# Optimization experiments

Measured on AMD Instinct MI355X. Metric: run time of the kernel, lower is better.

The kernel has to match this reference:

```python
import jax, jax.numpy as jnp
import numpy as np

MASK_NUM = -2.0**32 + 1.0  # additive masking constant from the original layer


def setup_inputs() -> dict:
    key = jax.random.key(0)
    k1, k2, k3, k4 = jax.random.split(key, 4)
    BH, S, D = 32, 2048, 64  # batch*heads, seq_len, head_dim
    B = 4                    # original batch (masks are per-batch, tiled by heads)
    queries = jax.random.normal(k1, (BH, S, D), dtype=jnp.float32)
    keys_ = jax.random.normal(k2, (BH, S, D), dtype=jnp.float32)
    values = jax.random.normal(k3, (BH, S, D), dtype=jnp.float32)
    masks = jax.random.randint(k4, (B, S), 0, 2, dtype=jnp.int32)
    return {"queries": queries, "keys": keys_, "values": values, "masks": masks}


def reference(queries, keys, values, masks):
    BH, S, D = queries.shape
    # scores = Q K^T / sqrt(D)   -> [BH, S, S]
    scores = jnp.einsum("bqd,bkd->bqk", queries, keys) / (D ** 0.5)
    # key-padding mask: masks [B, S] tiled along axis 0 by BH // B, broadcast over query dim
    reps = BH // masks.shape[0]
    m = jnp.tile(masks.astype(jnp.float32), (reps, 1))[:, None, :]  # [BH, 1, S]
    scores = scores + m * MASK_NUM
    # causal (future) mask: keep lower triangle, replace rest with MASK_NUM
    tril = jnp.tril(jnp.ones((S, S), dtype=jnp.float32))
    scores = jnp.where(tril == 0, jnp.float32(MASK_NUM), scores)
    attn = jax.nn.softmax(scores, axis=-1)
    # dropout_rate = 0.0 -> identity
    return jnp.einsum("bqk,bkd->bqd", attn, values)
```

## Files before the change

### kernel.cpp

```cpp
#include <hip/hip_runtime.h>

#define S_LEN 2048
#define HDIM  64
#define NHEAD 32
#define NBATCH 4
#define QBLK 64
#define KBLK 64
#define QK_SCALE (0.125f * 1.44269504088896341f)

typedef float f32x4 __attribute__((ext_vector_type(4)));
typedef short bf16x8 __attribute__((ext_vector_type(8)));

static __device__ __forceinline__ unsigned int cvt_pk_bf16(float lo, float hi) {
    unsigned int r;
    asm("v_cvt_pk_bf16_f32 %0, %1, %2" : "=v"(r) : "v"(lo), "v"(hi));
    return r;
}

__global__ void maskprep_kernel(const int* __restrict__ masks,
                                int* __restrict__ Lb,
                                unsigned long long* __restrict__ MB) {
    const int b = blockIdx.x;
    const int t = threadIdx.x;
    __shared__ int smin;
    if (t == 0) smin = S_LEN;
    __syncthreads();
    int local = S_LEN;
    for (int k = t; k < S_LEN; k += 64) {
        if (masks[b * S_LEN + k] == 0) { local = k; break; }
    }
    atomicMin(&smin, local);
    if (t < 32) {
        unsigned long long wbits = 0ull;
        for (int i = 0; i < 64; ++i)
            wbits |= (unsigned long long)(masks[b * S_LEN + t * 64 + i] & 1) << i;
        MB[b * 32 + t] = wbits;
    }
    __syncthreads();
    if (t == 0) Lb[b] = smin;
}

__global__ void meanv_kernel(const float* __restrict__ V, float* __restrict__ meanV) {
    const int bh = blockIdx.x;
    const int t = threadIdx.x;
    const int d = t & 63;
    const int part = t >> 6;
    const float* Vb = V + (size_t)bh * S_LEN * HDIM;
    float s = 0.f;
    const int k0 = part * (S_LEN / 4);
    for (int k = k0; k < k0 + S_LEN / 4; ++k) s += Vb[(size_t)k * HDIM + d];
    __shared__ float red[4][64];
    red[part][d] = s;
    __syncthreads();
    if (t < 64) {
        float tot = red[0][t] + red[1][t] + red[2][t] + red[3][t];
        meanV[bh * HDIM + t] = tot * (1.0f / (float)S_LEN);
    }
}

#define P_OFF 32768
#define LDSB  40960

__global__ __launch_bounds__(256) void attn_fwd(
    const float* __restrict__ Q, const float* __restrict__ K,
    const float* __restrict__ V, const float* __restrict__ meanV,
    const int* __restrict__ Lb, const unsigned long long* __restrict__ MB,
    float* __restrict__ out)
{
    __shared__ __align__(16) char lds[LDSB];
    const int tid  = threadIdx.x;
    const int lane = tid & 63;
    const int w    = tid >> 6;
    const int lq   = lane & 15;
    const int lk   = lane >> 4;

    const int bid  = blockIdx.x;
    const int nbid = (bid & 7) * 128 + (bid >> 3);
    const int bh   = nbid >> 5;
    const int qb   = 31 - (nbid & 31);
    const int q0   = qb * QBLK;
    const int b    = bh & (NBATCH - 1);
    const int nt   = qb + 1;

    const size_t ho = (size_t)bh * S_LEN * HDIM;
    const float* Qh = Q + ho;
    const float* Kh = K + ho;
    const float* Vh = V + ho;

    bf16x8 qf[2];
    {
        const float* qrow = Qh + (size_t)(q0 + w * 16 + lq) * HDIM;
        #pragma unroll
        for (int c = 0; c < 2; ++c) {
            const int d0 = lk * 8 + c * 32;
            float4 f0 = *(const float4*)(qrow + d0);
            float4 f1 = *(const float4*)(qrow + d0 + 4);
            int4 qi;
            qi.x = cvt_pk_bf16(f0.x * QK_SCALE, f0.y * QK_SCALE);
            qi.y = cvt_pk_bf16(f0.z * QK_SCALE, f0.w * QK_SCALE);
            qi.z = cvt_pk_bf16(f1.x * QK_SCALE, f1.y * QK_SCALE);
            qi.w = cvt_pk_bf16(f1.z * QK_SCALE, f1.w * QK_SCALE);
            qf[c] = *(bf16x8*)&qi;
        }
    }

    const int kr = tid >> 2;
    const int kc = (tid & 3) << 4;
    const float* Kp = Kh + (size_t)kr * HDIM + kc;
    const int vd = lane;
    const int vk = w * 16;
    const float* Vp = Vh + (size_t)vk * HDIM + vd;

    float4 ka0, ka1, ka2, ka3;
    float va[16];

    auto LOADKV = [&](int kk0) {
        const float4* kp = (const float4*)(Kp + (size_t)kk0 * HDIM);
        ka0 = kp[0]; ka1 = kp[1]; ka2 = kp[2]; ka3 = kp[3];
        const float* vp = Vp + (size_t)kk0 * HDIM;
        #pragma unroll
        for (int i = 0; i < 16; ++i) va[i] = vp[i * HDIM];
    };
    auto WRITEKV = [&](int bufbase) {
        int4 kv0, kv1;
        kv0.x = cvt_pk_bf16(ka0.x, ka0.y); kv0.y = cvt_pk_bf16(ka0.z, ka0.w);
        kv0.z = cvt_pk_bf16(ka1.x, ka1.y); kv0.w = cvt_pk_bf16(ka1.z, ka1.w);
        kv1.x = cvt_pk_bf16(ka2.x, ka2.y); kv1.y = cvt_pk_bf16(ka2.z, ka2.w);
        kv1.z = cvt_pk_bf16(ka3.x, ka3.y); kv1.w = cvt_pk_bf16(ka3.z, ka3.w);
        const int kswz = (kr & 7) << 4;
        *(int4*)&lds[bufbase + ((kr * 128 + kc * 2)      ^ kswz)] = kv0;
        *(int4*)&lds[bufbase + ((kr * 128 + kc * 2 + 16) ^ kswz)] = kv1;
        int4 vv0, vv1;
        vv0.x = cvt_pk_bf16(va[0],  va[1]);  vv0.y = cvt_pk_bf16(va[2],  va[3]);
        vv0.z = cvt_pk_bf16(va[4],  va[5]);  vv0.w = cvt_pk_bf16(va[6],  va[7]);
        vv1.x = cvt_pk_bf16(va[8],  va[9]);  vv1.y = cvt_pk_bf16(va[10], va[11]);
        vv1.z = cvt_pk_bf16(va[12], va[13]); vv1.w = cvt_pk_bf16(va[14], va[15]);
        const int vswz = (vd & 7) << 4;
        *(int4*)&lds[bufbase + 8192 + ((vd * 128 + vk * 2)      ^ vswz)] = vv0;
        *(int4*)&lds[bufbase + 8192 + ((vd * 128 + vk * 2 + 16) ^ vswz)] = vv1;
    };

    f32x4 acc[4];
    #pragma unroll
    for (int g = 0; g < 4; ++g) acc[g] = (f32x4){0.f, 0.f, 0.f, 0.f};
    float m_r = -__builtin_inff();
    float l_r = 0.f;

    const int swz = (lq & 7) << 4;
    const int pbase = P_OFF + (w << 11);
    const int wq = w * 16 + lq;

    LOADKV(0);
    WRITEKV(0);
    __syncthreads();

    for (int t = 0; t < nt; ++t) {
        const int cur = t & 1;
        const int kb  = cur << 14;
        const bool pre = (t + 1) < nt;
        if (pre) LOADKV((t + 1) * KBLK);

        f32x4 sacc[4];
        #pragma unroll
        for (int g = 0; g < 4; ++g) sacc[g] = (f32x4){0.f, 0.f, 0.f, 0.f};
        #pragma unroll
        for (int c = 0; c < 2; ++c) {
            #pragma unroll
            for (int g = 0; g < 4; ++g) {
                bf16x8 kf = *(const bf16x8*)&lds[kb + (((16 * g + lq) * 128 + 16 * lk + 64 * c) ^ swz)];
                sacc[g] = __builtin_amdgcn_mfma_f32_16x16x32_bf16(kf, qf[c], sacc[g], 0, 0, 0);
            }
        }

        const unsigned long long mb = MB[(b << 5) + t];
        const bool diag = (t == nt - 1);

        float mloc = sacc[0][0];
        #pragma unroll
        for (int g = 0; g < 4; ++g)
            #pragma unroll
            for (int r = 0; r < 4; ++r) mloc = fmaxf(mloc, sacc[g][r]);
        mloc = fmaxf(mloc, __shfl_xor(mloc, 16, 64));
        mloc = fmaxf(mloc, __shfl_xor(mloc, 32, 64));
        const float newm = fmaxf(m_r, mloc);
        const float sc = exp2f(m_r - newm);

        float ls = 0.f;
        #pragma unroll
        for (int g = 0; g < 4; ++g) {
            const unsigned int nib = (unsigned int)(mb >> (16 * g + 4 * lk)) & 0xFu;
            #pragma unroll
            for (int r = 0; r < 4; ++r) {
                const int kidx = 16 * g + 4 * lk + r;
                float e = exp2f(sacc[g][r] - newm);
                const bool kill = ((nib >> r) & 1u) || (diag && kidx > wq);
                e = kill ? 0.f : e;
                sacc[g][r] = e;
                ls += e;
            }
        }
        ls += __shfl_xor(ls, 16, 64);
        ls += __shfl_xor(ls, 32, 64);
        l_r = l_r * sc + ls;
        m_r = newm;

        float scb[4];
        #pragma unroll
        for (int r = 0; r < 4; ++r) scb[r] = __shfl(sc, 4 * lk + r, 64);
        #pragma unroll
        for (int g = 0; g < 4; ++g)
            #pragma unroll
            for (int r = 0; r < 4; ++r) acc[g][r] *= scb[r];

        #pragma unroll
        for (int g = 0; g < 4; ++g) {
            uint2 pw;
            pw.x = cvt_pk_bf16(sacc[g][0], sacc[g][1]);
            pw.y = cvt_pk_bf16(sacc[g][2], sacc[g][3]);
            *(uint2*)&lds[pbase + ((lq * 128 + 32 * g + 8 * lk) ^ swz)] = pw;
        }

        #pragma unroll
        for (int c = 0; c < 2; ++c) {
            bf16x8 pa = *(const bf16x8*)&lds[pbase + ((lq * 128 + 16 * lk + 64 * c) ^ swz)];
            #pragma unroll
            for (int g = 0; g < 4; ++g) {
                bf16x8 vb = *(const bf16x8*)&lds[kb + 8192 + (((lq + 16 * g) * 128 + 16 * lk + 64 * c) ^ swz)];
                acc[g] = __builtin_amdgcn_mfma_f32_16x16x32_bf16(pa, vb, acc[g], 0, 0, 0);
            }
        }

        if (pre) WRITEKV((cur ^ 1) << 14);
        __syncthreads();
    }

    const int myL = Lb[b];
    const float linv_s = 1.0f / l_r;
    float linv[4];
    #pragma unroll
    for (int r = 0; r < 4; ++r) linv[r] = __shfl(linv_s, 4 * lk + r, 64);
    #pragma unroll
    for (int r = 0; r < 4; ++r) {
        const int qrow = q0 + w * 16 + 4 * lk + r;
        float* orow = out + ho + (size_t)qrow * HDIM;
        if (qrow < myL) {
            #pragma unroll
            for (int g = 0; g < 4; ++g) orow[lq + 16 * g] = meanV[bh * HDIM + lq + 16 * g];
        } else {
            #pragma unroll
            for (int g = 0; g < 4; ++g) orow[lq + 16 * g] = acc[g][r] * linv[r];
        }
    }
}

extern "C" void kernel_launch(void* const* d_in, const int* in_sizes, int n_in,
                              void* d_out, int out_size, void* d_ws, size_t ws_size,
                              hipStream_t stream)
{
    const float* Q     = (const float*)d_in[0];
    const float* K     = (const float*)d_in[1];
    const float* V     = (const float*)d_in[2];
    const int*   masks = (const int*)d_in[3];
    float* out = (float*)d_out;

    float* meanV = (float*)d_ws;
    int*   Lb    = (int*)((char*)d_ws + 8192);
    unsigned long long* MB = (unsigned long long*)((char*)d_ws + 8208);

    maskprep_kernel<<<dim3(NBATCH), dim3(64), 0, stream>>>(masks, Lb, MB);
    meanv_kernel<<<dim3(NHEAD), dim3(256), 0, stream>>>(V, meanV);
    attn_fwd<<<dim3(1024), dim3(256), 0, stream>>>(Q, K, V, meanV, Lb, MB, out);
}
```

Measured before the change: 180.4 us.

## Pre-convert K/V to swizzled bf16, DMA to LDS, pair causal q-blocks

A separate kernel now converts K and V once to swizzled bf16 tile images in the workspace and computes meanV with atomics. The attention kernel stages those images straight into LDS with global_load_lds instead of loading fp32 per block and converting it. Each workgroup processes a short and a long causal q-block (j and 31-j) to balance work across 512 blocks. It also skips the softmax rescale when the running max grows by less than a threshold, raises wave priority around the MFMAs, and picks fully masked rows by l==0 instead of a prefix length. The costs are an extra pass over K and V, more workspace, and dependence on the workspace size for the fast path.

After: 155.5 us. 13.8% less time.

```diff
diff --git a/kernel.cpp b/kernel.cpp
--- a/kernel.cpp
+++ b/kernel.cpp
@@ -1,4 +1,5 @@
 #include <hip/hip_runtime.h>
+#include <stdint.h>
 
 #define S_LEN 2048
 #define HDIM  64
@@ -7,9 +8,17 @@
 #define QBLK 64
 #define KBLK 64
 #define QK_SCALE (0.125f * 1.44269504088896341f)
+#define DEFER_THR 8.0f
 
 typedef float f32x4 __attribute__((ext_vector_type(4)));
 typedef short bf16x8 __attribute__((ext_vector_type(8)));
+
+#define WS_MEANV 0
+#define WS_MB    8192
+#define WS_KBF   16384
+#define KVBYTES  (NHEAD * 32 * 8192)
+#define WS_VTBF  (WS_KBF + (size_t)KVBYTES)
+#define WS_NEED_PRE (WS_VTBF + (size_t)KVBYTES)
 
 static __device__ __forceinline__ unsigned int cvt_pk_bf16(float lo, float hi) {
     unsigned int r;
@@ -17,54 +26,101 @@
     return r;
 }
 
+static __device__ __forceinline__ void load_lds16(const void* g, void* l) {
+    __builtin_amdgcn_global_load_lds(
+        (const __attribute__((address_space(1))) uint32_t*)g,
+        (__attribute__((address_space(3))) uint32_t*)l, 16, 0, 0);
+}
+
 __global__ void maskprep_kernel(const int* __restrict__ masks,
-                                int* __restrict__ Lb,
                                 unsigned long long* __restrict__ MB) {
     const int b = blockIdx.x;
-    const int t = threadIdx.x;
-    __shared__ int smin;
-    if (t == 0) smin = S_LEN;
-    __syncthreads();
-    int local = S_LEN;
-    for (int k = t; k < S_LEN; k += 64) {
-        if (masks[b * S_LEN + k] == 0) { local = k; break; }
-    }
-    atomicMin(&smin, local);
-    if (t < 32) {
-        unsigned long long wbits = 0ull;
-        for (int i = 0; i < 64; ++i)
-            wbits |= (unsigned long long)(masks[b * S_LEN + t * 64 + i] & 1) << i;
-        MB[b * 32 + t] = wbits;
-    }
-    __syncthreads();
-    if (t == 0) Lb[b] = smin;
-}
-
-__global__ void meanv_kernel(const float* __restrict__ V, float* __restrict__ meanV) {
-    const int bh = blockIdx.x;
-    const int t = threadIdx.x;
-    const int d = t & 63;
-    const int part = t >> 6;
+    const int lane = threadIdx.x & 63;
+    const int w = threadIdx.x >> 6;
+    #pragma unroll
+    for (int i = 0; i < 8; ++i) {
+        const int word = i * 4 + w;
+        const int m = masks[b * S_LEN + word * 64 + lane];
+        const unsigned long long bits = __ballot(m != 0);
+        if (lane == 0) MB[b * 32 + word] = bits;
+    }
+}
+
+__global__ void meanv_atomic_kernel(const float* __restrict__ V, float* __restrict__ meanV) {
+    const int bh = blockIdx.x >> 3, part = blockIdx.x & 7;
+    const int t = threadIdx.x, d = t & 63, sub = t >> 6;
     const float* Vb = V + (size_t)bh * S_LEN * HDIM;
     float s = 0.f;
-    const int k0 = part * (S_LEN / 4);
-    for (int k = k0; k < k0 + S_LEN / 4; ++k) s += Vb[(size_t)k * HDIM + d];
+    const int k0 = part * 256 + sub * 64;
+    for (int k = k0; k < k0 + 64; ++k) s += Vb[(size_t)k * HDIM + d];
     __shared__ float red[4][64];
-    red[part][d] = s;
+    red[sub][d] = s;
     __syncthreads();
     if (t < 64) {
         float tot = red[0][t] + red[1][t] + red[2][t] + red[3][t];
-        meanV[bh * HDIM + t] = tot * (1.0f / (float)S_LEN);
+        atomicAdd(&meanV[bh * HDIM + t], tot * (1.0f / (float)S_LEN));
+    }
+}
+
+__global__ __launch_bounds__(256) void cvt_kernel(
+    const float* __restrict__ K, const float* __restrict__ V,
+    uint8_t* __restrict__ Kbf, uint8_t* __restrict__ Vtbf,
+    float* __restrict__ meanV)
+{
+    const int bh = blockIdx.x >> 5, t = blockIdx.x & 31;
+    const int tid = threadIdx.x, lane = tid & 63, w = tid >> 6;
+    const size_t ho = (size_t)bh * S_LEN * HDIM;
+    const size_t img = ((size_t)bh * 32 + t) * 8192;
+
+    {
+        const int kr = tid >> 2;
+        const int kc = (tid & 3) << 4;
+        const float4* kp = (const float4*)(K + ho + (size_t)(t * 64 + kr) * HDIM + kc);
+        float4 a0 = kp[0], a1 = kp[1], a2 = kp[2], a3 = kp[3];
+        int4 kv0, kv1;
+        kv0.x = cvt_pk_bf16(a0.x, a0.y); kv0.y = cvt_pk_bf16(a0.z, a0.w);
+        kv0.z = cvt_pk_bf16(a1.x, a1.y); kv0.w = cvt_pk_bf16(a1.z, a1.w);
+        kv1.x = cvt_pk_bf16(a2.x, a2.y); kv1.y = cvt_pk_bf16(a2.z, a2.w);
+        kv1.z = cvt_pk_bf16(a3.x, a3.y); kv1.w = cvt_pk_bf16(a3.z, a3.w);
+        const int swz = (kr & 7) << 4;
+        *(int4*)&Kbf[img + ((kr * 128 + kc * 2)      ^ swz)] = kv0;
+        *(int4*)&Kbf[img + ((kr * 128 + kc * 2 + 16) ^ swz)] = kv1;
+    }
+    {
+        const int vd = lane;
+        const int vk = w * 16;
+        const float* vp = V + ho + (size_t)(t * 64 + vk) * HDIM + vd;
+        float va[16];
+        float psum = 0.f;
+        #pragma unroll
+        for (int i = 0; i < 16; ++i) { va[i] = vp[(size_t)i * HDIM]; psum += va[i]; }
+        int4 vv0, vv1;
+        vv0.x = cvt_pk_bf16(va[0],  va[1]);  vv0.y = cvt_pk_bf16(va[2],  va[3]);
+        vv0.z = cvt_pk_bf16(va[4],  va[5]);  vv0.w = cvt_pk_bf16(va[6],  va[7]);
+        vv1.x = cvt_pk_bf16(va[8],  va[9]);  vv1.y = cvt_pk_bf16(va[10], va[11]);
+        vv1.z = cvt_pk_bf16(va[12], va[13]); vv1.w = cvt_pk_bf16(va[14], va[15]);
+        const int swz = (vd & 7) << 4;
+        *(int4*)&Vtbf[img + ((vd * 128 + vk * 2)      ^ swz)] = vv0;
+        *(int4*)&Vtbf[img + ((vd * 128 + vk * 2 + 16) ^ swz)] = vv1;
+        __shared__ float red[4][64];
+        red[w][vd] = psum;
+        __syncthreads();
+        if (tid < 64) {
+            float tot = red[0][tid] + red[1][tid] + red[2][tid] + red[3][tid];
+            atomicAdd(&meanV[bh * HDIM + tid], tot * (1.0f / (float)S_LEN));
+        }
     }
 }
 
 #define P_OFF 32768
 #define LDSB  40960
 
+template<bool PRE>
 __global__ __launch_bounds__(256) void attn_fwd(
     const float* __restrict__ Q, const float* __restrict__ K,
     const float* __restrict__ V, const float* __restrict__ meanV,
-    const int* __restrict__ Lb, const unsigned long long* __restrict__ MB,
+    const unsigned long long* __restrict__ MB,
+    const uint8_t* __restrict__ Kbf, const uint8_t* __restrict__ Vtbf,
     float* __restrict__ out)
 {
     __shared__ __align__(16) char lds[LDSB];
@@ -75,51 +131,41 @@
     const int lk   = lane >> 4;
 
     const int bid  = blockIdx.x;
-    const int nbid = (bid & 7) * 128 + (bid >> 3);
-    const int bh   = nbid >> 5;
-    const int qb   = 31 - (nbid & 31);
-    const int q0   = qb * QBLK;
+    const int nbid = (bid & 7) * 64 + (bid >> 3);
+    const int bh   = nbid >> 4;
+    const int j    = nbid & 15;
     const int b    = bh & (NBATCH - 1);
-    const int nt   = qb + 1;
 
     const size_t ho = (size_t)bh * S_LEN * HDIM;
     const float* Qh = Q + ho;
     const float* Kh = K + ho;
     const float* Vh = V + ho;
-
-    bf16x8 qf[2];
-    {
-        const float* qrow = Qh + (size_t)(q0 + w * 16 + lq) * HDIM;
-        #pragma unroll
-        for (int c = 0; c < 2; ++c) {
-            const int d0 = lk * 8 + c * 32;
-            float4 f0 = *(const float4*)(qrow + d0);
-            float4 f1 = *(const float4*)(qrow + d0 + 4);
-            int4 qi;
-            qi.x = cvt_pk_bf16(f0.x * QK_SCALE, f0.y * QK_SCALE);
-            qi.y = cvt_pk_bf16(f0.z * QK_SCALE, f0.w * QK_SCALE);
-            qi.z = cvt_pk_bf16(f1.x * QK_SCALE, f1.y * QK_SCALE);
-            qi.w = cvt_pk_bf16(f1.z * QK_SCALE, f1.w * QK_SCALE);
-            qf[c] = *(bf16x8*)&qi;
-        }
-    }
+    const uint8_t* kimg = Kbf  + (size_t)bh * 32 * 8192;
+    const uint8_t* vimg = Vtbf + (size_t)bh * 32 * 8192;
 
     const int kr = tid >> 2;
     const int kc = (tid & 3) << 4;
-    const float* Kp = Kh + (size_t)kr * HDIM + kc;
     const int vd = lane;
     const int vk = w * 16;
+    const float* Kp = Kh + (size_t)kr * HDIM + kc;
     const float* Vp = Vh + (size_t)vk * HDIM + vd;
-
     float4 ka0, ka1, ka2, ka3;
     float va[16];
 
+    auto STAGE = [&](int t, int bufbase) {
+        const uint8_t* gk = kimg + (size_t)t * 8192 + w * 2048 + lane * 16;
+        const uint8_t* gv = vimg + (size_t)t * 8192 + w * 2048 + lane * 16;
+        load_lds16(gk,        &lds[bufbase + w * 2048]);
+        load_lds16(gk + 1024, &lds[bufbase + w * 2048 + 1024]);
+        load_lds16(gv,        &lds[bufbase + 8192 + w * 2048]);
+        load_lds16(gv + 1024, &lds[bufbase + 8192 + w * 2048 + 1024]);
+    };
     auto LOADKV = [&](int kk0) {
         const float4* kp = (const float4*)(Kp + (size_t)kk0 * HDIM);
         ka0 = kp[0]; ka1 = kp[1]; ka2 = kp[2]; ka3 = kp[3];
         const float* vp = Vp + (size_t)kk0 * HDIM;
         #pragma unroll
-        for (int i = 0; i < 16; ++i) va[i] = vp[i * HDIM];
+        for (int i = 0; i < 16; ++i) va[i] = vp[(size_t)i * HDIM];
     };
     auto WRITEKV = [&](int bufbase) {
         int4 kv0, kv1;
@@ -140,115 +186,146 @@
         *(int4*)&lds[bufbase + 8192 + ((vd * 128 + vk * 2 + 16) ^ vswz)] = vv1;
     };
 
-    f32x4 acc[4];
-    #pragma unroll
-    for (int g = 0; g < 4; ++g) acc[g] = (f32x4){0.f, 0.f, 0.f, 0.f};
-    float m_r = -__builtin_inff();
-    float l_r = 0.f;
-
     const int swz = (lq & 7) << 4;
     const int pbase = P_OFF + (w << 11);
     const int wq = w * 16 + lq;
 
-    LOADKV(0);
-    WRITEKV(0);
-    __syncthreads();
-
-    for (int t = 0; t < nt; ++t) {
-        const int cur = t & 1;
-        const int kb  = cur << 14;
-        const bool pre = (t + 1) < nt;
-        if (pre) LOADKV((t + 1) * KBLK);
-
-        f32x4 sacc[4];
-        #pragma unroll
-        for (int g = 0; g < 4; ++g) sacc[g] = (f32x4){0.f, 0.f, 0.f, 0.f};
-        #pragma unroll
-        for (int c = 0; c < 2; ++c) {
+    #pragma unroll 1
+    for (int pass = 0; pass < 2; ++pass) {
+        const int qb = pass ? (31 - j) : j;
+        const int q0 = qb * QBLK;
+        const int nt = qb + 1;
+
+        bf16x8 qf[2];
+        {
+            const float* qrow = Qh + (size_t)(q0 + w * 16 + lq) * HDIM;
+            #pragma unroll
+            for (int c = 0; c < 2; ++c) {
+                const int d0 = lk * 8 + c * 32;
+                float4 f0 = *(const float4*)(qrow + d0);
+                float4 f1 = *(const float4*)(qrow + d0 + 4);
+                int4 qi;
+                qi.x = cvt_pk_bf16(f0.x * QK_SCALE, f0.y * QK_SCALE);
+                qi.y = cvt_pk_bf16(f0.z * QK_SCALE, f0.w * QK_SCALE);
+                qi.z = cvt_pk_bf16(f1.x * QK_SCALE, f1.y * QK_SCALE);
+                qi.w = cvt_pk_bf16(f1.z * QK_SCALE, f1.w * QK_SCALE);
+                qf[c] = *(bf16x8*)&qi;
+            }
+        }
+
+        f32x4 acc[4];
+        #pragma unroll
+        for (int g = 0; g < 4; ++g) acc[g] = (f32x4){0.f, 0.f, 0.f, 0.f};
+        float m_r = -__builtin_inff();
+        float l_r = 0.f;
+
+        if constexpr (PRE) STAGE(0, 0);
+        else { LOADKV(0); WRITEKV(0); }
+        __syncthreads();
+
+        for (int t = 0; t < nt; ++t) {
+            const int cur = t & 1;
+            const int kb  = cur << 14;
+            const bool pre = (t + 1) < nt;
+            if constexpr (PRE) { if (pre) STAGE(t + 1, (cur ^ 1) << 14); }
+            else               { if (pre) LOADKV((t + 1) * KBLK); }
+
+            f32x4 sacc[4];
+            #pragma unroll
+            for (int g = 0; g < 4; ++g) sacc[g] = (f32x4){0.f, 0.f, 0.f, 0.f};
+            __builtin_amdgcn_s_setprio(1);
+            #pragma unroll
+            for (int c = 0; c < 2; ++c) {
+                #pragma unroll
+                for (int g = 0; g < 4; ++g) {
+                    bf16x8 kf = *(const bf16x8*)&lds[kb + (((16 * g + lq) * 128 + 16 * lk + 64 * c) ^ swz)];
+                    sacc[g] = __builtin_amdgcn_mfma_f32_16x16x32_bf16(kf, qf[c], sacc[g], 0, 0, 0);
+                }
+            }
+            __builtin_amdgcn_s_setprio(0);
+
+            const unsigned long long mb = MB[(b << 5) + t];
+            const bool diag = (t == nt - 1);
+
+            float mloc = sacc[0][0];
+            #pragma unroll
+            for (int g = 0; g < 4; ++g)
+                #pragma unroll
+                for (int r = 0; r < 4; ++r) mloc = fmaxf(mloc, sacc[g][r]);
+            mloc = fmaxf(mloc, __shfl_xor(mloc, 16, 64));
+            mloc = fmaxf(mloc, __shfl_xor(mloc, 32, 64));
+
+            if (!__all(mloc - m_r <= DEFER_THR)) {
+                const float newm = fmaxf(m_r, mloc);
+                const float sc = exp2f(m_r - newm);
+                l_r *= sc;
+                m_r = newm;
+                float scb[4];
+                #pragma unroll
+                for (int r = 0; r < 4; ++r) scb[r] = __shfl(sc, 4 * lk + r, 64);
+                #pragma unroll
+                for (int g = 0; g < 4; ++g)
+                    #pragma unroll
+                    for (int r = 0; r < 4; ++r) acc[g][r] *= scb[r];
+            }
+
+            float ls = 0.f;
             #pragma unroll
             for (int g = 0; g < 4; ++g) {
-                bf16x8 kf = *(const bf16x8*)&lds[kb + (((16 * g + lq) * 128 + 16 * lk + 64 * c) ^ swz)];
-                sacc[g] = __builtin_amdgcn_mfma_f32_16x16x32_bf16(kf, qf[c], sacc[g], 0, 0, 0);
-            }
+                const unsigned int nib = (unsigned int)(mb >> (16 * g + 4 * lk)) & 0xFu;
+                #pragma unroll
+                for (int r = 0; r < 4; ++r) {
+                    const int kidx = 16 * g + 4 * lk + r;
+                    float e = exp2f(sacc[g][r] - m_r);
+                    const bool kill = ((nib >> r) & 1u) || (diag && kidx > wq);
+                    e = kill ? 0.f : e;
+                    sacc[g][r] = e;
+                    ls += e;
+                }
+            }
+            ls += __shfl_xor(ls, 16, 64);
+            ls += __shfl_xor(ls, 32, 64);
+            l_r += ls;
+
+            #pragma unroll
+            for (int g = 0; g < 4; ++g) {
+                uint2 pw;
+                pw.x = cvt_pk_bf16(sacc[g][0], sacc[g][1]);
+                pw.y = cvt_pk_bf16(sacc[g][2], sacc[g][3]);
+                *(uint2*)&lds[pbase + ((lq * 128 + 32 * g + 8 * lk) ^ swz)] = pw;
+            }
+
+            __builtin_amdgcn_s_setprio(1);
+            #pragma unroll
+            for (int c = 0; c < 2; ++c) {
+                bf16x8 pa = *(const bf16x8*)&lds[pbase + ((lq * 128 + 16 * lk + 64 * c) ^ swz)];
+                #pragma unroll
+                for (int g = 0; g < 4; ++g) {
+                    bf16x8 vb = *(const bf16x8*)&lds[kb + 8192 + (((lq + 16 * g) * 128 + 16 * lk + 64 * c) ^ swz)];
+                    acc[g] = __builtin_amdgcn_mfma_f32_16x16x32_bf16(pa, vb, acc[g], 0, 0, 0);
+                }
+            }
+            __builtin_amdgcn_s_setprio(0);
+
+            if constexpr (!PRE) { if (pre) WRITEKV((cur ^ 1) << 14); }
+            __syncthreads();
         }
 
-        const unsigned long long mb = MB[(b << 5) + t];
-        const bool diag = (t == nt - 1);
-
-        float mloc = sacc[0][0];
-        #pragma unroll
-        for (int g = 0; g < 4; ++g)
-            #pragma unroll
-            for (int r = 0; r < 4; ++r) mloc = fmaxf(mloc, sacc[g][r]);
-        mloc = fmaxf(mloc, __shfl_xor(mloc, 16, 64));
-        mloc = fmaxf(mloc, __shfl_xor(mloc, 32, 64));
-        const float newm = fmaxf(m_r, mloc);
-        const float sc = exp2f(m_r - newm);
-
-        float ls = 0.f;
-        #pragma unroll
-        for (int g = 0; g < 4; ++g) {
-            const unsigned int nib = (unsigned int)(mb >> (16 * g + 4 * lk)) & 0xFu;
-            #pragma unroll
-            for (int r = 0; r < 4; ++r) {
-                const int kidx = 16 * g + 4 * lk + r;
-                float e = exp2f(sacc[g][r] - newm);
-                const bool kill = ((nib >> r) & 1u) || (diag && kidx > wq);
-                e = kill ? 0.f : e;
-                sacc[g][r] = e;
-                ls += e;
-            }
-        }
-        ls += __shfl_xor(ls, 16, 64);
-        ls += __shfl_xor(ls, 32, 64);
-        l_r = l_r * sc + ls;
-        m_r = newm;
-
-        float scb[4];
-        #pragma unroll
-        for (int r = 0; r < 4; ++r) scb[r] = __shfl(sc, 4 * lk + r, 64);
-        #pragma unroll
-        for (int g = 0; g < 4; ++g)
-            #pragma unroll
-            for (int r = 0; r < 4; ++r) acc[g][r] *= scb[r];
-
-        #pragma unroll
-        for (int g = 0; g < 4; ++g) {
-            uint2 pw;
-            pw.x = cvt_pk_bf16(sacc[g][0], sacc[g][1]);
-            pw.y = cvt_pk_bf16(sacc[g][2], sacc[g][3]);
-            *(uint2*)&lds[pbase + ((lq * 128 + 32 * g + 8 * lk) ^ swz)] = pw;
-        }
-
-        #pragma unroll
-        for (int c = 0; c < 2; ++c) {
-            bf16x8 pa = *(const bf16x8*)&lds[pbase + ((lq * 128 + 16 * lk + 64 * c) ^ swz)];
-            #pragma unroll
-            for (int g = 0; g < 4; ++g) {
-                bf16x8 vb = *(const bf16x8*)&lds[kb + 8192 + (((lq + 16 * g) * 128 + 16 * lk + 64 * c) ^ swz)];
-                acc[g] = __builtin_amdgcn_mfma_f32_16x16x32_bf16(pa, vb, acc[g], 0, 0, 0);
-            }
-        }
-
-        if (pre) WRITEKV((cur ^ 1) << 14);
-        __syncthreads();
-    }
-
-    const int myL = Lb[b];
-    const float linv_s = 1.0f / l_r;
-    float linv[4];
-    #pragma unroll
-    for (int r = 0; r < 4; ++r) linv[r] = __shfl(linv_s, 4 * lk + r, 64);
-    #pragma unroll
-    for (int r = 0; r < 4; ++r) {
-        const int qrow = q0 + w * 16 + 4 * lk + r;
-        float* orow = out + ho + (size_t)qrow * HDIM;
-        if (qrow < myL) {
-            #pragma unroll
-            for (int g = 0; g < 4; ++g) orow[lq + 16 * g] = meanV[bh * HDIM + lq + 16 * g];
-        } else {
-            #pragma unroll
-            for (int g = 0; g < 4; ++g) orow[lq + 16 * g] = acc[g][r] * linv[r];
+        float lr_b[4];
+        #pragma unroll
+        for (int r = 0; r < 4; ++r) lr_b[r] = __shfl(l_r, 4 * lk + r, 64);
+        #pragma unroll
+        for (int r = 0; r < 4; ++r) {
+            const int qrow = q0 + w * 16 + 4 * lk + r;
+            float* orow = out + ho + (size_t)qrow * HDIM;
+            if (lr_b[r] == 0.f) {
+                #pragma unroll
+                for (int g = 0; g < 4; ++g) orow[lq + 16 * g] = meanV[bh * HDIM + lq + 16 * g];
+            } else {
+                const float inv = 1.0f / lr_b[r];
+                #pragma unroll
+                for (int g = 0; g < 4; ++g) orow[lq + 16 * g] = acc[g][r] * inv;
+            }
         }
     }
 }
@@ -263,11 +340,20 @@
     const int*   masks = (const int*)d_in[3];
     float* out = (float*)d_out;
 
-    float* meanV = (float*)d_ws;
-    int*   Lb    = (int*)((char*)d_ws + 8192);
-    unsigned long long* MB = (unsigned long long*)((char*)d_ws + 8208);
-
-    maskprep_kernel<<<dim3(NBATCH), dim3(64), 0, stream>>>(masks, Lb, MB);
-    meanv_kernel<<<dim3(NHEAD), dim3(256), 0, stream>>>(V, meanV);
-    attn_fwd<<<dim3(1024), dim3(256), 0, stream>>>(Q, K, V, meanV, Lb, MB, out);
-}
+    char* ws = (char*)d_ws;
+    float* meanV = (float*)(ws + WS_MEANV);
+    unsigned long long* MB = (unsigned long long*)(ws + WS_MB);
+
+    hipMemsetAsync(meanV, 0, NHEAD * HDIM * sizeof(float), stream);
+    maskprep_kernel<<<dim3(NBATCH), dim3(256), 0, stream>>>(masks, MB);
+
+    if (ws_size >= WS_NEED_PRE) {
+        uint8_t* Kbf  = (uint8_t*)(ws + WS_KBF);
+        uint8_t* Vtbf = (uint8_t*)(ws + WS_VTBF);
+        cvt_kernel<<<dim3(NHEAD * 32), dim3(256), 0, stream>>>(K, V, Kbf, Vtbf, meanV);
+        attn_fwd<true><<<dim3(512), dim3(256), 0, stream>>>(Q, K, V, meanV, MB, Kbf, Vtbf, out);
+    } else {
+        meanv_atomic_kernel<<<dim3(256), dim3(256), 0, stream>>>(V, meanV);
+        attn_fwd<false><<<dim3(512), dim3(256), 0, stream>>>(Q, K, V, meanV, MB, nullptr, nullptr, out);
+    }
+}
```
